# Performance work log

Measured on AMD Instinct MI355X. Metric: run time of the kernel, lower is better.

## Reference

```python
import jax, jax.numpy as jnp
import numpy as np

B, T, D = 4, 4096, 64

def setup_inputs() -> dict:
    key = jax.random.key(0)
    kq, kk, kv = jax.random.split(key, 3)
    Q = jax.random.normal(kq, (B, T, D), dtype=jnp.float32)
    K = jax.random.normal(kk, (B, T, D), dtype=jnp.float32)
    V = jax.random.normal(kv, (B, T, D), dtype=jnp.float32)
    mask = jnp.zeros((B, T, T), dtype=jnp.float32)
    return {"Q": Q, "K": K, "V": V, "mask": mask}

def reference(Q, K, V, mask):
    dk = Q.shape[-1]
    # NOTE: original scales by 1/dk (not 1/sqrt(dk)) -- reproduce faithfully.
    scores = jnp.einsum('btd,bsd->bts', Q, K) * (1.0 / dk)  # [B,T,T]
    scores = scores + mask
    attn = jax.nn.softmax(scores, axis=-1)
    return jnp.einsum('bts,bsd->btd', attn, V)  # [B,T,D]
```

## Files before the change

### kernel.cpp

```cpp
#include <hip/hip_runtime.h>
#include <stdint.h>

#define BB 4
#define TT 4096
#define DD 64
#define QBLK 32
#define KBLK 64
#define NIT (TT / KBLK)

typedef short short8 __attribute__((ext_vector_type(8)));
typedef float f32x4 __attribute__((ext_vector_type(4)));

__device__ __forceinline__ uint16_t f2bf(float x) {
  uint32_t u = __float_as_uint(x);
  u += 0x7FFFu + ((u >> 16) & 1u);
  return (uint16_t)(u >> 16);
}
__device__ __forceinline__ float bf2f(uint16_t h) {
  return __uint_as_float(((uint32_t)h) << 16);
}

#define MFMA(a, b, c) __builtin_amdgcn_mfma_f32_16x16x32_bf16((a), (b), (c), 0, 0, 0)

__global__ __launch_bounds__(256) void prep_kernel(
    const float* __restrict__ Q, const float* __restrict__ K, const float* __restrict__ V,
    uint16_t* __restrict__ Qh, uint16_t* __restrict__ Ql,
    uint16_t* __restrict__ Kh, uint16_t* __restrict__ Kl,
    uint16_t* __restrict__ Vh, uint16_t* __restrict__ Vl) {
  __shared__ float vt[64][65];
  const int blk = blockIdx.x;
  const int b = blk >> 6;
  const int r0 = (blk & 63) << 6;
  const int t = threadIdx.x;
  const size_t base = ((size_t)b * TT + r0) * DD;
  for (int i = t; i < 64 * 64; i += 256) {
    float q = Q[base + i] * 0.015625f;
    uint16_t h = f2bf(q);
    Qh[base + i] = h;
    Ql[base + i] = f2bf(q - bf2f(h));
    float k = K[base + i];
    h = f2bf(k);
    Kh[base + i] = h;
    Kl[base + i] = f2bf(k - bf2f(h));
    int r = i >> 6, c = i & 63;
    vt[r][c] = V[base + i];
  }
  __syncthreads();
  for (int i = t; i < 64 * 64; i += 256) {
    int d = i >> 6, c = i & 63;
    float v = vt[c][d];
    uint16_t h = f2bf(v);
    size_t o = ((size_t)b * DD + d) * TT + r0 + c;
    Vh[o] = h;
    Vl[o] = f2bf(v - bf2f(h));
  }
}

__global__ __launch_bounds__(128) void attn_kernel(
    const float* __restrict__ mask, float* __restrict__ out,
    const uint16_t* __restrict__ Qh, const uint16_t* __restrict__ Ql,
    const uint16_t* __restrict__ Kh, const uint16_t* __restrict__ Kl,
    const uint16_t* __restrict__ Vh, const uint16_t* __restrict__ Vl) {
  __shared__ uint16_t Kh_s[64][72], Kl_s[64][72];
  __shared__ uint16_t Vh_s[64][72], Vl_s[64][72];
  __shared__ uint16_t Ph_s[2][16][72], Pl_s[2][16][72];

  const int blk = blockIdx.x;
  const int xcd = blk & 7;
  const int b = xcd >> 1;
  const int qtile = ((blk >> 3) << 1) | (xcd & 1);
  const int q0 = qtile * QBLK;
  const int t = threadIdx.x;
  const int w = t >> 6;
  const int l = t & 63;
  const int lr = l & 15;
  const int lq = l >> 4;

  const uint16_t* qhp = Qh + ((size_t)b * TT + q0 + w * 16 + lr) * DD + lq * 8;
  const uint16_t* qlp = Ql + ((size_t)b * TT + q0 + w * 16 + lr) * DD + lq * 8;
  short8 qh[2], ql[2];
  qh[0] = *(const short8*)(qhp);
  qh[1] = *(const short8*)(qhp + 32);
  ql[0] = *(const short8*)(qlp);
  ql[1] = *(const short8*)(qlp + 32);

  f32x4 o[4];
  float mrow[4], lrow[4];
#pragma unroll
  for (int dt = 0; dt < 4; ++dt) o[dt] = (f32x4){0.f, 0.f, 0.f, 0.f};
#pragma unroll
  for (int j = 0; j < 4; ++j) { mrow[j] = -1e30f; lrow[j] = 0.f; }

  const float* mp[4];
#pragma unroll
  for (int j = 0; j < 4; ++j)
    mp[j] = mask + ((size_t)b * TT + q0 + w * 16 + lq * 4 + j) * TT + lr;

  float mk[16];
#pragma unroll
  for (int tt = 0; tt < 4; ++tt)
#pragma unroll
    for (int j = 0; j < 4; ++j)
      mk[tt * 4 + j] = __builtin_nontemporal_load(mp[j] + tt * 16);

  const size_t kvb = (size_t)b * TT * DD;
  const size_t vtb = (size_t)b * DD * TT;

  for (int it = 0; it < NIT; ++it) {
    const int s0 = it * KBLK;
    __syncthreads();
#pragma unroll
    for (int i = 0; i < 4; ++i) {
      const int idx = i * 128 + t;
      const int row = idx >> 3, c = idx & 7;
      const size_t ko = kvb + (size_t)(s0 + row) * DD + c * 8;
      *(short8*)&Kh_s[row][c * 8] = *(const short8*)(Kh + ko);
      *(short8*)&Kl_s[row][c * 8] = *(const short8*)(Kl + ko);
      const size_t vo = vtb + (size_t)row * TT + s0 + c * 8;
      *(short8*)&Vh_s[row][c * 8] = *(const short8*)(Vh + vo);
      *(short8*)&Vl_s[row][c * 8] = *(const short8*)(Vl + vo);
    }
    __syncthreads();

    float mk2[16];
    if (it + 1 < NIT) {
#pragma unroll
      for (int tt = 0; tt < 4; ++tt)
#pragma unroll
        for (int j = 0; j < 4; ++j)
          mk2[tt * 4 + j] = __builtin_nontemporal_load(mp[j] + (s0 + KBLK) + tt * 16);
    } else {
#pragma unroll
      for (int i = 0; i < 16; ++i) mk2[i] = 0.f;
    }

    f32x4 s[4];
#pragma unroll
    for (int tt = 0; tt < 4; ++tt) {
      f32x4 acc = (f32x4){0.f, 0.f, 0.f, 0.f};
#pragma unroll
      for (int c = 0; c < 2; ++c) {
        const short8 bh = *(const short8*)&Kh_s[tt * 16 + lr][c * 32 + lq * 8];
        const short8 bl = *(const short8*)&Kl_s[tt * 16 + lr][c * 32 + lq * 8];
        acc = MFMA(qh[c], bh, acc);
        acc = MFMA(ql[c], bh, acc);
        acc = MFMA(qh[c], bl, acc);
      }
      s[tt] = acc;
    }
#pragma unroll
    for (int tt = 0; tt < 4; ++tt)
#pragma unroll
      for (int j = 0; j < 4; ++j) s[tt][j] += mk[tt * 4 + j];

    float cm[4];
#pragma unroll
    for (int j = 0; j < 4; ++j)
      cm[j] = fmaxf(fmaxf(s[0][j], s[1][j]), fmaxf(s[2][j], s[3][j]));
#pragma unroll
    for (int d = 1; d < 16; d <<= 1)
#pragma unroll
      for (int j = 0; j < 4; ++j) cm[j] = fmaxf(cm[j], __shfl_xor(cm[j], d, 16));
    float scl[4];
#pragma unroll
    for (int j = 0; j < 4; ++j) {
      const float mn = fmaxf(mrow[j], cm[j]);
      scl[j] = __expf(mrow[j] - mn);
      mrow[j] = mn;
    }
#pragma unroll
    for (int tt = 0; tt < 4; ++tt)
#pragma unroll
      for (int j = 0; j < 4; ++j) s[tt][j] = __expf(s[tt][j] - mrow[j]);
    float rs[4];
#pragma unroll
    for (int j = 0; j < 4; ++j) rs[j] = (s[0][j] + s[1][j]) + (s[2][j] + s[3][j]);
#pragma unroll
    for (int d = 1; d < 16; d <<= 1)
#pragma unroll
      for (int j = 0; j < 4; ++j) rs[j] += __shfl_xor(rs[j], d, 16);
#pragma unroll
    for (int j = 0; j < 4; ++j) lrow[j] = lrow[j] * scl[j] + rs[j];
#pragma unroll
    for (int dt = 0; dt < 4; ++dt)
#pragma unroll
      for (int j = 0; j < 4; ++j) o[dt][j] *= scl[j];

#pragma unroll
    for (int tt = 0; tt < 4; ++tt)
#pragma unroll
      for (int j = 0; j < 4; ++j) {
        const float p = s[tt][j];
        const uint16_t h = f2bf(p);
        Ph_s[w][lq * 4 + j][tt * 16 + lr] = h;
        Pl_s[w][lq * 4 + j][tt * 16 + lr] = f2bf(p - bf2f(h));
      }

#pragma unroll
    for (int c = 0; c < 2; ++c) {
      const short8 ph = *(const short8*)&Ph_s[w][lr][c * 32 + lq * 8];
      const short8 pl = *(const short8*)&Pl_s[w][lr][c * 32 + lq * 8];
#pragma unroll
      for (int dt = 0; dt < 4; ++dt) {
        const short8 vh = *(const short8*)&Vh_s[dt * 16 + lr][c * 32 + lq * 8];
        const short8 vl = *(const short8*)&Vl_s[dt * 16 + lr][c * 32 + lq * 8];
        o[dt] = MFMA(ph, vh, o[dt]);
        o[dt] = MFMA(pl, vh, o[dt]);
        o[dt] = MFMA(ph, vl, o[dt]);
      }
    }

#pragma unroll
    for (int i = 0; i < 16; ++i) mk[i] = mk2[i];
  }

#pragma unroll
  for (int j = 0; j < 4; ++j) {
    const float inv = 1.0f / lrow[j];
    const size_t ob = ((size_t)b * TT + q0 + w * 16 + lq * 4 + j) * DD + lr;
#pragma unroll
    for (int dt = 0; dt < 4; ++dt) out[ob + dt * 16] = o[dt][j] * inv;
  }
}

extern "C" void kernel_launch(void* const* d_in, const int* in_sizes, int n_in,
                              void* d_out, int out_size, void* d_ws, size_t ws_size,
                              hipStream_t stream) {
  const float* Q = (const float*)d_in[0];
  const float* K = (const float*)d_in[1];
  const float* V = (const float*)d_in[2];
  const float* mask = (const float*)d_in[3];
  float* out = (float*)d_out;

  const size_t NE = (size_t)BB * TT * DD;
  uint16_t* ws = (uint16_t*)d_ws;
  uint16_t* Qh = ws;
  uint16_t* Ql = ws + NE;
  uint16_t* Kh = ws + 2 * NE;
  uint16_t* Kl = ws + 3 * NE;
  uint16_t* Vh = ws + 4 * NE;
  uint16_t* Vl = ws + 5 * NE;

  prep_kernel<<<dim3(256), dim3(256), 0, stream>>>(Q, K, V, Qh, Ql, Kh, Kl, Vh, Vl);
  attn_kernel<<<dim3(512), dim3(128), 0, stream>>>(mask, out, Qh, Ql, Kh, Kl, Vh, Vl);
}
```

Baseline: 484.9 us.

## Split key sequence into segments with larger blocks and a combine pass

Restructures attention as a split-K (flash-decoding style) computation: each block now handles 128 query rows with 8 waves over one of up to 4 key segments. Partial outputs and row max/sum go to workspace, and a separate combine kernel merges them. Larger blocks let more waves reuse each K/V tile loaded into shared memory, which cuts redundant K/V global traffic. In exchange it adds partial-result writes, an extra kernel launch, and a reduction pass, and the number of segments depends on how much workspace is available.

Result: faster. 422.5 us (-12.9%).

```diff
diff --git a/kernel.cpp b/kernel.cpp
--- a/kernel.cpp
+++ b/kernel.cpp
@@ -4,9 +4,7 @@
 #define BB 4
 #define TT 4096
 #define DD 64
-#define QBLK 32
 #define KBLK 64
-#define NIT (TT / KBLK)
 
 typedef short short8 __attribute__((ext_vector_type(8)));
 typedef float f32x4 __attribute__((ext_vector_type(4)));
@@ -56,28 +54,39 @@
   }
 }
 
-__global__ __launch_bounds__(128) void attn_kernel(
+template <int NSEG, int NW>
+__global__ __launch_bounds__(NW * 64, 4) void attn_kernel(
     const float* __restrict__ mask, float* __restrict__ out,
+    float* __restrict__ Op, float* __restrict__ Mp, float* __restrict__ Lp,
     const uint16_t* __restrict__ Qh, const uint16_t* __restrict__ Ql,
     const uint16_t* __restrict__ Kh, const uint16_t* __restrict__ Kl,
     const uint16_t* __restrict__ Vh, const uint16_t* __restrict__ Vl) {
+  constexpr int RPB = NW * 16;
+  constexpr int PBH = (TT / RPB) / 2;
+  constexpr int SEGLEN = TT / NSEG;
+  constexpr int NIT = SEGLEN / KBLK;
+
   __shared__ uint16_t Kh_s[64][72], Kl_s[64][72];
   __shared__ uint16_t Vh_s[64][72], Vl_s[64][72];
-  __shared__ uint16_t Ph_s[2][16][72], Pl_s[2][16][72];
-
-  const int blk = blockIdx.x;
-  const int xcd = blk & 7;
+  __shared__ uint16_t Ph_s[NW][16][72], Pl_s[NW][16][72];
+
+  const int bid = blockIdx.x;
+  const int xcd = bid & 7;
   const int b = xcd >> 1;
-  const int qtile = ((blk >> 3) << 1) | (xcd & 1);
-  const int q0 = qtile * QBLK;
+  const int u = bid >> 3;
+  const int rbl = (u % PBH) * 2 + (xcd & 1);
+  const int seg = u / PBH;
+  const int q0 = rbl * RPB;
   const int t = threadIdx.x;
   const int w = t >> 6;
   const int l = t & 63;
   const int lr = l & 15;
   const int lq = l >> 4;
-
-  const uint16_t* qhp = Qh + ((size_t)b * TT + q0 + w * 16 + lr) * DD + lq * 8;
-  const uint16_t* qlp = Ql + ((size_t)b * TT + q0 + w * 16 + lr) * DD + lq * 8;
+  const int qrow = q0 + w * 16;
+  const int sb = seg * SEGLEN;
+
+  const uint16_t* qhp = Qh + ((size_t)b * TT + qrow + lr) * DD + lq * 8;
+  const uint16_t* qlp = Ql + ((size_t)b * TT + qrow + lr) * DD + lq * 8;
   short8 qh[2], ql[2];
   qh[0] = *(const short8*)(qhp);
   qh[1] = *(const short8*)(qhp + 32);
@@ -94,7 +103,7 @@
   const float* mp[4];
 #pragma unroll
   for (int j = 0; j < 4; ++j)
-    mp[j] = mask + ((size_t)b * TT + q0 + w * 16 + lq * 4 + j) * TT + lr;
+    mp[j] = mask + ((size_t)b * TT + qrow + lq * 4 + j) * TT + sb + lr;
 
   float mk[16];
 #pragma unroll
@@ -107,12 +116,10 @@
   const size_t vtb = (size_t)b * DD * TT;
 
   for (int it = 0; it < NIT; ++it) {
-    const int s0 = it * KBLK;
+    const int s0 = sb + it * KBLK;
     __syncthreads();
-#pragma unroll
-    for (int i = 0; i < 4; ++i) {
-      const int idx = i * 128 + t;
-      const int row = idx >> 3, c = idx & 7;
+    for (int i = t; i < 512; i += NW * 64) {
+      const int row = i >> 3, c = i & 7;
       const size_t ko = kvb + (size_t)(s0 + row) * DD + c * 8;
       *(short8*)&Kh_s[row][c * 8] = *(const short8*)(Kh + ko);
       *(short8*)&Kl_s[row][c * 8] = *(const short8*)(Kl + ko);
@@ -128,7 +135,7 @@
       for (int tt = 0; tt < 4; ++tt)
 #pragma unroll
         for (int j = 0; j < 4; ++j)
-          mk2[tt * 4 + j] = __builtin_nontemporal_load(mp[j] + (s0 + KBLK) + tt * 16);
+          mk2[tt * 4 + j] = __builtin_nontemporal_load(mp[j] + (it + 1) * KBLK + tt * 16);
     } else {
 #pragma unroll
       for (int i = 0; i < 16; ++i) mk2[i] = 0.f;
@@ -214,13 +221,41 @@
     for (int i = 0; i < 16; ++i) mk[i] = mk2[i];
   }
 
-#pragma unroll
-  for (int j = 0; j < 4; ++j) {
-    const float inv = 1.0f / lrow[j];
-    const size_t ob = ((size_t)b * TT + q0 + w * 16 + lq * 4 + j) * DD + lr;
-#pragma unroll
-    for (int dt = 0; dt < 4; ++dt) out[ob + dt * 16] = o[dt][j] * inv;
-  }
+  if constexpr (NSEG == 1) {
+#pragma unroll
+    for (int j = 0; j < 4; ++j) {
+      const float inv = 1.0f / lrow[j];
+      const size_t ob = ((size_t)b * TT + qrow + lq * 4 + j) * DD + lr;
+#pragma unroll
+      for (int dt = 0; dt < 4; ++dt) out[ob + dt * 16] = o[dt][j] * inv;
+    }
+  } else {
+    const int grow = b * TT + qrow + lq * 4;
+#pragma unroll
+    for (int j = 0; j < 4; ++j) {
+      const size_t r = (size_t)seg * (BB * TT) + grow + j;
+#pragma unroll
+      for (int dt = 0; dt < 4; ++dt) Op[r * 64 + dt * 16 + lr] = o[dt][j];
+      if (lr == 0) { Mp[r] = mrow[j]; Lp[r] = lrow[j]; }
+    }
+  }
+}
+
+__global__ __launch_bounds__(256) void combine_kernel(
+    const float* __restrict__ Op, const float* __restrict__ Mp,
+    const float* __restrict__ Lp, float* __restrict__ out, int nseg) {
+  const int gid = blockIdx.x * 256 + threadIdx.x;
+  const int r = gid >> 6, d = gid & 63;
+  constexpr int ROWS = BB * TT;
+  float m = -3.0e38f;
+  for (int s = 0; s < nseg; ++s) m = fmaxf(m, Mp[s * ROWS + r]);
+  float num = 0.f, den = 0.f;
+  for (int s = 0; s < nseg; ++s) {
+    const float e = __expf(Mp[s * ROWS + r] - m);
+    den += Lp[s * ROWS + r] * e;
+    num += Op[((size_t)s * ROWS + r) * 64 + d] * e;
+  }
+  out[(size_t)r * 64 + d] = num / den;
 }
 
 extern "C" void kernel_launch(void* const* d_in, const int* in_sizes, int n_in,
@@ -233,6 +268,7 @@
   float* out = (float*)d_out;
 
   const size_t NE = (size_t)BB * TT * DD;
+  const size_t ROWS = (size_t)BB * TT;
   uint16_t* ws = (uint16_t*)d_ws;
   uint16_t* Qh = ws;
   uint16_t* Ql = ws + NE;
@@ -241,6 +277,29 @@
   uint16_t* Vh = ws + 4 * NE;
   uint16_t* Vl = ws + 5 * NE;
 
+  const size_t bf_bytes = 6 * NE * 2;
+  const size_t per_seg = ROWS * 64 * 4 + ROWS * 2 * 4;
+  int nseg = (ws_size >= bf_bytes + 4 * per_seg) ? 4
+           : (ws_size >= bf_bytes + 2 * per_seg) ? 2 : 1;
+
+  char* pbase = (char*)d_ws + bf_bytes;
+  float* Op = (float*)pbase;
+  float* Mp = (float*)(pbase + (size_t)nseg * ROWS * 64 * 4);
+  float* Lp = Mp + (size_t)nseg * ROWS;
+
   prep_kernel<<<dim3(256), dim3(256), 0, stream>>>(Q, K, V, Qh, Ql, Kh, Kl, Vh, Vl);
-  attn_kernel<<<dim3(512), dim3(128), 0, stream>>>(mask, out, Qh, Ql, Kh, Kl, Vh, Vl);
-}
+
+  if (nseg == 4) {
+    attn_kernel<4, 8><<<dim3(512), dim3(512), 0, stream>>>(
+        mask, out, Op, Mp, Lp, Qh, Ql, Kh, Kl, Vh, Vl);
+  } else if (nseg == 2) {
+    attn_kernel<2, 8><<<dim3(256), dim3(512), 0, stream>>>(
+        mask, out, Op, Mp, Lp, Qh, Ql, Kh, Kl, Vh, Vl);
+  } else {
+    attn_kernel<1, 4><<<dim3(256), dim3(256), 0, stream>>>(
+        mask, out, Op, Mp, Lp, Qh, Ql, Kh, Kl, Vh, Vl);
+  }
+  if (nseg > 1) {
+    combine_kernel<<<dim3((ROWS * 64) / 256), dim3(256), 0, stream>>>(Op, Mp, Lp, out, nseg);
+  }
+}
```
